# Optimization experiments

Measured on AMD Instinct MI355X. Metric: run time of the kernel, lower is better.

## Reference

```python
import jax, jax.numpy as jnp
import numpy as np

DIM = 512
NUM_HEADS = 16
HEAD_DIM = DIM // NUM_HEADS
WH, WW = 7, 7
N = WH * WW  # 49 tokens per window
B_ = 4096    # num_windows * batch
TABLE = (2 * WH - 1) * (2 * WW - 1)  # 169


def _make_rel_pos_index():
    # Swin-style relative position index over a Wh x Ww window
    coords_h = np.arange(WH)
    coords_w = np.arange(WW)
    coords = np.stack(np.meshgrid(coords_h, coords_w, indexing='ij'))  # [2, Wh, Ww]
    coords_flat = coords.reshape(2, -1)                                # [2, N]
    rel = coords_flat[:, :, None] - coords_flat[:, None, :]            # [2, N, N]
    rel = rel.transpose(1, 2, 0).astype(np.int32)                      # [N, N, 2]
    rel[:, :, 0] += WH - 1
    rel[:, :, 1] += WW - 1
    rel[:, :, 0] *= 2 * WW - 1
    return rel.sum(-1)  # [N, N] values in [0, TABLE)


def setup_inputs() -> dict:
    key = jax.random.key(0)
    ks = jax.random.split(key, 6)
    s_in = 1.0 / np.sqrt(DIM)
    return {
        'x': jax.random.normal(ks[0], (B_, N, DIM), jnp.float32),
        'qkv_w': jax.random.normal(ks[1], (DIM, 3 * DIM), jnp.float32) * s_in,
        'qkv_b': jnp.zeros((3 * DIM,), jnp.float32),
        'proj_w': jax.random.normal(ks[2], (DIM, DIM), jnp.float32) * s_in,
        'proj_b': jnp.zeros((DIM,), jnp.float32),
        'rel_bias_table': jax.random.normal(ks[3], (TABLE, NUM_HEADS), jnp.float32) * 0.02,
        'rel_pos_index': jnp.asarray(_make_rel_pos_index(), jnp.int32),
    }


def reference(x, qkv_w, qkv_b, proj_w, proj_b, rel_bias_table, rel_pos_index):
    B, n, C = x.shape
    scale = HEAD_DIM ** (-0.5)
    qkv = x @ qkv_w + qkv_b                                   # [B, N, 3C]
    qkv = qkv.reshape(B, n, 3, NUM_HEADS, HEAD_DIM)
    q, k, v = (qkv[:, :, i].transpose(0, 2, 1, 3) for i in range(3))  # [B, H, N, d]
    attn = jnp.einsum('bhnd,bhmd->bhnm', q * scale, k)        # [B, H, N, N]
    # relative position bias gather: [N, N, H] -> [1, H, N, N]
    bias = rel_bias_table[rel_pos_index]                      # [N, N, H]
    attn = attn + bias.transpose(2, 0, 1)[None]
    attn = jax.nn.softmax(attn, axis=-1)
    out = jnp.einsum('bhnm,bhmd->bhnd', attn, v)              # [B, H, N, d]
    out = out.transpose(0, 2, 1, 3).reshape(B, n, C)
    return out @ proj_w + proj_b
```

## Files before the change

kernel.cpp:

```cpp
#include <hip/hip_runtime.h>
#include <hip/hip_bf16.h>
#include <cstdint>
#include <cstdio>

#define M_TOK   200704
#define DIM     512
#define QKV_N   1536
#define NWIN    4096
#define NTOK    49
#define NHEAD   16
#define HD      32
#define TABLE_N 169

typedef float  f32x4  __attribute__((ext_vector_type(4)));
typedef __bf16 bf16x8 __attribute__((ext_vector_type(8)));

__device__ __forceinline__ unsigned short f2bf(float f) {
  union { float f; unsigned u; } v; v.f = f;
  unsigned r = (v.u + 0x7FFFu + ((v.u >> 16) & 1u)) >> 16;
  return (unsigned short)r;
}

__global__ __launch_bounds__(256) void prep_kernel(
    const float* __restrict__ qkv_w, const float* __restrict__ proj_w,
    const float* __restrict__ table, const int* __restrict__ rel_idx,
    unsigned short* __restrict__ Wt, unsigned short* __restrict__ Pt,
    float* __restrict__ biasFull)
{
  int i = blockIdx.x * 256 + threadIdx.x;
  if (i < 786432) {
    int n = i >> 9, k = i & 511;
    Wt[i] = f2bf(qkv_w[(size_t)k * 1536 + n]);
  } else if (i < 786432 + 262144) {
    int j = i - 786432;
    int n = j >> 9, k = j & 511;
    Pt[j] = f2bf(proj_w[(size_t)k * 512 + n]);
  } else if (i < 786432 + 262144 + NHEAD * NTOK * NTOK) {
    int j = i - 1048576;
    int h = j / (NTOK * NTOK), r = j % (NTOK * NTOK);
    biasFull[j] = table[(size_t)rel_idx[r] * NHEAD + h];
  }
}

template<bool AF32, bool CF32>
__global__ __launch_bounds__(256) void gemm_bt(
    const void* __restrict__ Ap, const unsigned short* __restrict__ Bt,
    const float* __restrict__ bias, void* __restrict__ Cp,
    int M, int N, int K)
{
  __shared__ unsigned short As[128 * 32];
  __shared__ unsigned short Bs[128 * 32];
  const int tid  = threadIdx.x;
  const int lane = tid & 63;
  const int wave = tid >> 6;
  const int quad = lane >> 4, l16 = lane & 15;
  const int wm = (wave >> 1) * 64, wn = (wave & 1) * 64;
  const size_t m0 = (size_t)blockIdx.y * 128;
  const size_t n0 = (size_t)blockIdx.x * 128;

  f32x4 acc[4][4] = {};

  const float*          Af = (const float*)Ap;
  const unsigned short* Ah = (const unsigned short*)Ap;

  for (int kb = 0; kb < K; kb += 32) {
    if (AF32) {
      #pragma unroll
      for (int pass = 0; pass < 4; ++pass) {
        int r  = pass * 32 + (tid >> 3);
        int c4 = (tid & 7) * 4;
        float4 u = *(const float4*)(Af + (m0 + r) * (size_t)K + kb + c4);
        union { unsigned short s[4]; uint2 v; } pk;
        pk.s[0] = f2bf(u.x); pk.s[1] = f2bf(u.y);
        pk.s[2] = f2bf(u.z); pk.s[3] = f2bf(u.w);
        *(uint2*)(&As[r * 32 + c4]) = pk.v;
      }
    } else {
      #pragma unroll
      for (int half = 0; half < 2; ++half) {
        int r  = half * 64 + (tid >> 2);
        int c8 = (tid & 3) * 8;
        *(uint4*)(&As[r * 32 + c8]) =
            *(const uint4*)(Ah + (m0 + r) * (size_t)K + kb + c8);
      }
    }
    #pragma unroll
    for (int half = 0; half < 2; ++half) {
      int r  = half * 64 + (tid >> 2);
      int c8 = (tid & 3) * 8;
      *(uint4*)(&Bs[r * 32 + c8]) =
          *(const uint4*)(Bt + (n0 + r) * (size_t)K + kb + c8);
    }
    __syncthreads();

    bf16x8 afr[4], bfr[4];
    #pragma unroll
    for (int mt = 0; mt < 4; ++mt)
      afr[mt] = *(const bf16x8*)(&As[(wm + mt * 16 + l16) * 32 + quad * 8]);
    #pragma unroll
    for (int nt = 0; nt < 4; ++nt)
      bfr[nt] = *(const bf16x8*)(&Bs[(wn + nt * 16 + l16) * 32 + quad * 8]);
    #pragma unroll
    for (int mt = 0; mt < 4; ++mt)
      #pragma unroll
      for (int nt = 0; nt < 4; ++nt)
        acc[mt][nt] = __builtin_amdgcn_mfma_f32_16x16x32_bf16(
            afr[mt], bfr[nt], acc[mt][nt], 0, 0, 0);
    __syncthreads();
  }

  float bcol[4];
  #pragma unroll
  for (int nt = 0; nt < 4; ++nt) bcol[nt] = bias[n0 + wn + nt * 16 + l16];
  float*          Cf = (float*)Cp;
  unsigned short* Ch = (unsigned short*)Cp;
  #pragma unroll
  for (int mt = 0; mt < 4; ++mt)
    #pragma unroll
    for (int r = 0; r < 4; ++r) {
      size_t row = m0 + wm + mt * 16 + quad * 4 + r;
      #pragma unroll
      for (int nt = 0; nt < 4; ++nt) {
        size_t col = n0 + wn + nt * 16 + l16;
        float v = acc[mt][nt][r] + bcol[nt];
        if (CF32) Cf[row * (size_t)N + col] = v;
        else      Ch[row * (size_t)N + col] = f2bf(v);
      }
    }
}

__global__ __launch_bounds__(256) void attn_kernel(
    const unsigned short* __restrict__ qkv,
    const float* __restrict__ biasFull,
    unsigned short* __restrict__ attn_out)
{
  const int b    = blockIdx.x >> 2;
  const int qh   = blockIdx.x & 3;
  const int wave = threadIdx.x >> 6;
  const int h    = qh * 4 + wave;
  const int lane = threadIdx.x & 63;
  const int quad = lane >> 4, l16 = lane & 15;

  __shared__ unsigned short smem[4 * 6144];
  unsigned short* wbase = smem + wave * 6144;
  unsigned short* Qs = wbase;
  unsigned short* Ks = wbase + 2048;
  unsigned short* Vt = wbase + 4096;
  unsigned short* Ps = wbase;

  const size_t rowb = (size_t)b * NTOK;

  #pragma unroll
  for (int seg = 0; seg < 4; ++seg) {
    int t  = seg * 16 + (lane >> 2);
    int c8 = (lane & 3) * 8;
    uint4 zq = {0, 0, 0, 0}, zk = {0, 0, 0, 0}, zv = {0, 0, 0, 0};
    if (t < NTOK) {
      const unsigned short* g = qkv + (rowb + t) * 1536 + h * 32 + c8;
      zq = *(const uint4*)(g);
      zk = *(const uint4*)(g + 512);
      zv = *(const uint4*)(g + 1024);
    }
    *(uint4*)(Qs + t * 32 + c8) = zq;
    *(uint4*)(Ks + t * 32 + c8) = zk;
    union { uint4 v; unsigned short s[8]; } uv; uv.v = zv;
    #pragma unroll
    for (int j = 0; j < 8; ++j) Vt[(c8 + j) * 64 + t] = uv.s[j];
  }

  f32x4 sacc[4][4] = {};
  {
    bf16x8 aq[4], ak[4];
    #pragma unroll
    for (int mt = 0; mt < 4; ++mt)
      aq[mt] = *(const bf16x8*)(Qs + (mt * 16 + l16) * 32 + quad * 8);
    #pragma unroll
    for (int nt = 0; nt < 4; ++nt)
      ak[nt] = *(const bf16x8*)(Ks + (nt * 16 + l16) * 32 + quad * 8);
    #pragma unroll
    for (int mt = 0; mt < 4; ++mt)
      #pragma unroll
      for (int nt = 0; nt < 4; ++nt)
        sacc[mt][nt] = __builtin_amdgcn_mfma_f32_16x16x32_bf16(
            aq[mt], ak[nt], sacc[mt][nt], 0, 0, 0);
  }

  const float scale = 0.17677669529663687f;
  const float* bh = biasFull + h * (NTOK * NTOK);
  #pragma unroll
  for (int mt = 0; mt < 4; ++mt) {
    #pragma unroll
    for (int r = 0; r < 4; ++r) {
      int m = mt * 16 + quad * 4 + r;
      float v[4];
      #pragma unroll
      for (int nt = 0; nt < 4; ++nt) {
        int n = nt * 16 + l16;
        float s = sacc[mt][nt][r] * scale;
        if (m < NTOK && n < NTOK) s += bh[m * NTOK + n];
        v[nt] = (n < NTOK) ? s : -1e30f;
      }
      float mx = fmaxf(fmaxf(v[0], v[1]), fmaxf(v[2], v[3]));
      #pragma unroll
      for (int off = 1; off <= 8; off <<= 1) mx = fmaxf(mx, __shfl_xor(mx, off, 64));
      float e[4], sum = 0.f;
      #pragma unroll
      for (int nt = 0; nt < 4; ++nt) { e[nt] = __expf(v[nt] - mx); sum += e[nt]; }
      #pragma unroll
      for (int off = 1; off <= 8; off <<= 1) sum += __shfl_xor(sum, off, 64);
      float inv = 1.0f / sum;
      #pragma unroll
      for (int nt = 0; nt < 4; ++nt)
        Ps[m * 64 + nt * 16 + l16] = f2bf(e[nt] * inv);
    }
  }

  f32x4 oacc[4][2] = {};
  #pragma unroll
  for (int kt = 0; kt < 2; ++kt) {
    bf16x8 ap[4], av[2];
    #pragma unroll
    for (int mt = 0; mt < 4; ++mt)
      ap[mt] = *(const bf16x8*)(Ps + (mt * 16 + l16) * 64 + kt * 32 + quad * 8);
    #pragma unroll
    for (int dt = 0; dt < 2; ++dt)
      av[dt] = *(const bf16x8*)(Vt + (dt * 16 + l16) * 64 + kt * 32 + quad * 8);
    #pragma unroll
    for (int mt = 0; mt < 4; ++mt)
      #pragma unroll
      for (int dt = 0; dt < 2; ++dt)
        oacc[mt][dt] = __builtin_amdgcn_mfma_f32_16x16x32_bf16(
            ap[mt], av[dt], oacc[mt][dt], 0, 0, 0);
  }

  #pragma unroll
  for (int mt = 0; mt < 4; ++mt)
    #pragma unroll
    for (int r = 0; r < 4; ++r) {
      int m = mt * 16 + quad * 4 + r;
      if (m < NTOK) {
        #pragma unroll
        for (int dt = 0; dt < 2; ++dt)
          attn_out[(rowb + m) * 512 + h * 32 + dt * 16 + l16] =
              f2bf(oacc[mt][dt][r]);
      }
    }
}

#define WS_QKV   0ull
#define WS_ATTN  616562688ull
#define WS_WT    822083584ull
#define WS_PT    823656448ull
#define WS_BIAS  824180736ull
#define WS_END   824334400ull

extern "C" void kernel_launch(void* const* d_in, const int* in_sizes, int n_in,
                              void* d_out, int out_size, void* d_ws, size_t ws_size,
                              hipStream_t stream) {
  const float* x       = (const float*)d_in[0];
  const float* qkv_w   = (const float*)d_in[1];
  const float* qkv_b   = (const float*)d_in[2];
  const float* proj_w  = (const float*)d_in[3];
  const float* proj_b  = (const float*)d_in[4];
  const float* table   = (const float*)d_in[5];
  const int*   rel_idx = (const int*)d_in[6];
  float* out = (float*)d_out;

  if (ws_size < WS_END) {
    fprintf(stderr, "kernel_launch: ws_size %zu < needed %llu\n", ws_size, WS_END);
    return;
  }
  char* ws = (char*)d_ws;
  unsigned short* qkv   = (unsigned short*)(ws + WS_QKV);
  unsigned short* attnb = (unsigned short*)(ws + WS_ATTN);
  unsigned short* Wt    = (unsigned short*)(ws + WS_WT);
  unsigned short* Pt    = (unsigned short*)(ws + WS_PT);
  float*          biasF = (float*)(ws + WS_BIAS);

  prep_kernel<<<4247, 256, 0, stream>>>(qkv_w, proj_w, table, rel_idx, Wt, Pt, biasF);

  dim3 g1(QKV_N / 128, M_TOK / 128);
  gemm_bt<true, false><<<g1, 256, 0, stream>>>(x, Wt, qkv_b, qkv, M_TOK, QKV_N, DIM);

  attn_kernel<<<NWIN * 4, 256, 0, stream>>>(qkv, biasF, attnb);

  dim3 g2(DIM / 128, M_TOK / 128);
  gemm_bt<false, true><<<g2, 256, 0, stream>>>(attnb, Pt, proj_b, out, M_TOK, DIM, DIM);
}
```

Baseline: 1.743 ms.

## Pre-cast input to bf16, use direct global-to-LDS loads and XCD-aware block swizzle

Adds a separate cast kernel that converts x to bf16 once into workspace (reusing the attention buffer), so the QKV GEMM no longer converts fp32 in its inner loop and re-reads fp32 x for each of 12 N-tiles. The GEMM tile loads now use global_load_lds to write straight into shared memory without going through registers. Blocks are remapped so neighbouring tiles land on the same XCD for better L2 reuse. The cost is an extra pass over x (read fp32, write bf16).

```diff
diff --git a/kernel.cpp b/kernel.cpp
--- a/kernel.cpp
+++ b/kernel.cpp
@@ -19,6 +19,27 @@
   union { float f; unsigned u; } v; v.f = f;
   unsigned r = (v.u + 0x7FFFu + ((v.u >> 16) & 1u)) >> 16;
   return (unsigned short)r;
+}
+
+__device__ __forceinline__ void gload_lds16(const void* gsrc, void* ldst) {
+  __builtin_amdgcn_global_load_lds(
+      (const __attribute__((address_space(1))) void*)gsrc,
+      (__attribute__((address_space(3))) void*)ldst,
+      16, 0, 0);
+}
+
+__global__ __launch_bounds__(256) void cast_kernel(
+    const float* __restrict__ x, unsigned short* __restrict__ xb)
+{
+  size_t i = ((size_t)blockIdx.x * 256 + threadIdx.x) * 8;
+  float4 a = *(const float4*)(x + i);
+  float4 b = *(const float4*)(x + i + 4);
+  union { unsigned short s[8]; uint4 v; } pk;
+  pk.s[0] = f2bf(a.x); pk.s[1] = f2bf(a.y);
+  pk.s[2] = f2bf(a.z); pk.s[3] = f2bf(a.w);
+  pk.s[4] = f2bf(b.x); pk.s[5] = f2bf(b.y);
+  pk.s[6] = f2bf(b.z); pk.s[7] = f2bf(b.w);
+  *(uint4*)(xb + i) = pk.v;
 }
 
 __global__ __launch_bounds__(256) void prep_kernel(
@@ -42,9 +63,9 @@
   }
 }
 
-template<bool AF32, bool CF32>
+template<bool CF32>
 __global__ __launch_bounds__(256) void gemm_bt(
-    const void* __restrict__ Ap, const unsigned short* __restrict__ Bt,
+    const unsigned short* __restrict__ A, const unsigned short* __restrict__ Bt,
     const float* __restrict__ bias, void* __restrict__ Cp,
     int M, int N, int K)
 {
@@ -55,41 +76,25 @@
   const int wave = tid >> 6;
   const int quad = lane >> 4, l16 = lane & 15;
   const int wm = (wave >> 1) * 64, wn = (wave & 1) * 64;
-  const size_t m0 = (size_t)blockIdx.y * 128;
-  const size_t n0 = (size_t)blockIdx.x * 128;
+
+  const unsigned nwg  = gridDim.x * gridDim.y;
+  const unsigned flat = blockIdx.y * gridDim.x + blockIdx.x;
+  const unsigned cpx  = nwg >> 3;
+  const unsigned swz  = (flat & 7u) * cpx + (flat >> 3);
+  const size_t n0 = (size_t)(swz % gridDim.x) * 128;
+  const size_t m0 = (size_t)(swz / gridDim.x) * 128;
 
   f32x4 acc[4][4] = {};
 
-  const float*          Af = (const float*)Ap;
-  const unsigned short* Ah = (const unsigned short*)Ap;
-
   for (int kb = 0; kb < K; kb += 32) {
-    if (AF32) {
-      #pragma unroll
-      for (int pass = 0; pass < 4; ++pass) {
-        int r  = pass * 32 + (tid >> 3);
-        int c4 = (tid & 7) * 4;
-        float4 u = *(const float4*)(Af + (m0 + r) * (size_t)K + kb + c4);
-        union { unsigned short s[4]; uint2 v; } pk;
-        pk.s[0] = f2bf(u.x); pk.s[1] = f2bf(u.y);
-        pk.s[2] = f2bf(u.z); pk.s[3] = f2bf(u.w);
-        *(uint2*)(&As[r * 32 + c4]) = pk.v;
-      }
-    } else {
-      #pragma unroll
-      for (int half = 0; half < 2; ++half) {
-        int r  = half * 64 + (tid >> 2);
-        int c8 = (tid & 3) * 8;
-        *(uint4*)(&As[r * 32 + c8]) =
-            *(const uint4*)(Ah + (m0 + r) * (size_t)K + kb + c8);
-      }
-    }
-    #pragma unroll
-    for (int half = 0; half < 2; ++half) {
-      int r  = half * 64 + (tid >> 2);
-      int c8 = (tid & 3) * 8;
-      *(uint4*)(&Bs[r * 32 + c8]) =
-          *(const uint4*)(Bt + (n0 + r) * (size_t)K + kb + c8);
+    #pragma unroll
+    for (int p = 0; p < 2; ++p) {
+      int c = p * 256 + tid;
+      int r = c >> 2, c8 = (c & 3) * 8;
+      gload_lds16(A  + (m0 + r) * (size_t)K + kb + c8,
+                  &As[(p * 256 + wave * 64) * 8]);
+      gload_lds16(Bt + (n0 + r) * (size_t)K + kb + c8,
+                  &Bs[(p * 256 + wave * 64) * 8]);
     }
     __syncthreads();
 
@@ -273,17 +278,20 @@
   char* ws = (char*)d_ws;
   unsigned short* qkv   = (unsigned short*)(ws + WS_QKV);
   unsigned short* attnb = (unsigned short*)(ws + WS_ATTN);
+  unsigned short* xb    = (unsigned short*)(ws + WS_ATTN);
   unsigned short* Wt    = (unsigned short*)(ws + WS_WT);
   unsigned short* Pt    = (unsigned short*)(ws + WS_PT);
   float*          biasF = (float*)(ws + WS_BIAS);
 
+  cast_kernel<<<50176, 256, 0, stream>>>(x, xb);
+
   prep_kernel<<<4247, 256, 0, stream>>>(qkv_w, proj_w, table, rel_idx, Wt, Pt, biasF);
 
   dim3 g1(QKV_N / 128, M_TOK / 128);
-  gemm_bt<true, false><<<g1, 256, 0, stream>>>(x, Wt, qkv_b, qkv, M_TOK, QKV_N, DIM);
+  gemm_bt<false><<<g1, 256, 0, stream>>>(xb, Wt, qkv_b, qkv, M_TOK, QKV_N, DIM);
 
   attn_kernel<<<NWIN * 4, 256, 0, stream>>>(qkv, biasF, attnb);
 
   dim3 g2(DIM / 128, M_TOK / 128);
-  gemm_bt<false, true><<<g2, 256, 0, stream>>>(attnb, Pt, proj_b, out, M_TOK, DIM, DIM);
-}
+  gemm_bt<true><<<g2, 256, 0, stream>>>(attnb, Pt, proj_b, out, M_TOK, DIM, DIM);
+}
```

New measurement: 1.676 ms. 3.9% less time.
